# Performance work log

Measured on AMD Instinct MI355X. Metric: run time of the kernel, lower is better.

Reference implementation:

```python
import jax, jax.numpy as jnp
import numpy as np

B, T, C, H = 2048, 128, 256, 64

def setup_inputs() -> dict:
    key = jax.random.key(0)
    kx, kk, kq, kv = jax.random.split(key, 4)
    s = 1.0 / np.sqrt(C)  # nn.Linear default init scale (approx)
    return {
        "x": jax.random.normal(kx, (B, T, C), dtype=jnp.float32),
        "Wk": jax.random.uniform(kk, (C, H), jnp.float32, -s, s),
        "Wq": jax.random.uniform(kq, (C, H), jnp.float32, -s, s),
        "Wv": jax.random.uniform(kv, (C, H), jnp.float32, -s, s),
    }

def reference(x, Wk, Wq, Wv):
    # x: [B,T,C]; projections to [B,T,H]
    k = jnp.einsum('btc,ch->bth', x, Wk)
    q = jnp.einsum('btc,ch->bth', x, Wq)
    v = jnp.einsum('btc,ch->bth', x, Wv)
    # NOTE: original scales by C**-0.5 (input dim), not head_size**-0.5
    scale = jnp.asarray(C, x.dtype) ** -0.5
    wei = jnp.einsum('bth,bsh->bts', q, k) * scale  # [B,T,T]
    causal = jnp.tril(jnp.ones((T, T), dtype=bool))
    wei = jnp.where(causal, wei, -jnp.inf)
    wei = jax.nn.softmax(wei, axis=-1)
    # dropout is identity in eval mode (deterministic reference)
    return jnp.einsum('bts,bsh->bth', wei, v)
```

## Files before the change

kernel.cpp:

```cpp
#include <hip/hip_runtime.h>

typedef __bf16 bf16;
typedef __bf16 bf16x4 __attribute__((ext_vector_type(4)));
typedef __bf16 bf16x8 __attribute__((ext_vector_type(8)));
typedef float  f32x4  __attribute__((ext_vector_type(4)));

#define B_ 2048
#define T_ 128
#define C_ 256
#define H_ 64

#define SMEM_BYTES 54272

__global__ void wt_kernel(const float* __restrict__ Wk, const float* __restrict__ Wq,
                          const float* __restrict__ Wv, bf16* __restrict__ Wt) {
    int o = blockIdx.x * 256 + threadIdx.x;
    int slot = o >> 14;
    int r    = o & 16383;
    int cc   = r >> 6;
    int h    = r & 63;
    const float* src = (slot == 0) ? Wq : (slot == 1 ? Wk : Wv);
    Wt[slot * 16384 + h * 256 + cc] = (bf16)src[r];
}

__global__ void __launch_bounds__(256, 3)
attn_kernel(const float* __restrict__ xg, const bf16* __restrict__ Wt,
            float* __restrict__ outg) {
    __shared__ __align__(16) char smem_raw[SMEM_BYTES];
    bf16* Qs  = (bf16*)smem_raw;
    bf16* Ks  = (bf16*)(smem_raw + 18432);
    bf16* Vt  = (bf16*)(smem_raw + 36864);
    bf16* Ps  = (bf16*)smem_raw;

    const int tid  = threadIdx.x;
    const int b    = blockIdx.x;
    const int w    = tid >> 6;
    const int lane = tid & 63;
    const int quad = lane >> 4;
    const int n16  = lane & 15;

    const f32x4 zero4 = {0.f, 0.f, 0.f, 0.f};
    const float*  xbp = xg + (size_t)b * (T_ * C_);
    const ushort* WtU = (const ushort*)Wt;

    f32x4 acc[2][12];
    #pragma unroll
    for (int mt = 0; mt < 2; mt++)
        #pragma unroll
        for (int nt = 0; nt < 12; nt++) acc[mt][nt] = zero4;

    #pragma unroll
    for (int ks = 0; ks < 8; ks++) {
        bf16x8 a[2];
        #pragma unroll
        for (int mt = 0; mt < 2; mt++) {
            const float* ap = xbp + (16 * (2 * w + mt) + n16) * C_ + ks * 32 + 8 * quad;
            float4 a0 = *(const float4*)(ap);
            float4 a1 = *(const float4*)(ap + 4);
            bf16x8 av = {(bf16)a0.x, (bf16)a0.y, (bf16)a0.z, (bf16)a0.w,
                         (bf16)a1.x, (bf16)a1.y, (bf16)a1.z, (bf16)a1.w};
            a[mt] = av;
        }
        #pragma unroll
        for (int nt = 0; nt < 12; nt++) {
            const ushort* wp = WtU + (nt >> 2) * 16384 + (16 * (nt & 3) + n16) * 256 + ks * 32 + 8 * quad;
            bf16x8 bfr = *(const bf16x8*)wp;
            acc[0][nt] = __builtin_amdgcn_mfma_f32_16x16x32_bf16(a[0], bfr, acc[0][nt], 0, 0, 0);
            acc[1][nt] = __builtin_amdgcn_mfma_f32_16x16x32_bf16(a[1], bfr, acc[1][nt], 0, 0, 0);
        }
    }

    #pragma unroll
    for (int mt = 0; mt < 2; mt++) {
        int tbase = 16 * (2 * w + mt) + 4 * quad;
        #pragma unroll
        for (int nt = 0; nt < 4; nt++) {
            int h = 16 * nt + n16;
            #pragma unroll
            for (int r = 0; r < 4; r++)
                Qs[(tbase + r) * 72 + h] = (bf16)(acc[mt][nt][r] * 0.0625f);
        }
        #pragma unroll
        for (int nt = 4; nt < 8; nt++) {
            int h = 16 * (nt & 3) + n16;
            #pragma unroll
            for (int r = 0; r < 4; r++)
                Ks[(tbase + r) * 72 + h] = (bf16)acc[mt][nt][r];
        }
        #pragma unroll
        for (int nt = 8; nt < 12; nt++) {
            int h = 16 * (nt - 8) + n16;
            bf16x4 pv = {(bf16)acc[mt][nt][0], (bf16)acc[mt][nt][1],
                         (bf16)acc[mt][nt][2], (bf16)acc[mt][nt][3]};
            *(bf16x4*)(Vt + h * 136 + tbase) = pv;
        }
    }
    __syncthreads();

    f32x4 sacc[2][8];
    int mts[2] = {w, 7 - w};
    #pragma unroll
    for (int half = 0; half < 2; half++) {
        int mt = mts[half];
        int sT = ((mt >> 1) + 1) * 2;
        bf16x8 qa[2];
        #pragma unroll
        for (int ks = 0; ks < 2; ks++)
            qa[ks] = *(const bf16x8*)(Qs + (16 * mt + n16) * 72 + 32 * ks + 8 * quad);
        #pragma unroll
        for (int nt = 0; nt < 8; nt++) {
            sacc[half][nt] = zero4;
            if (nt < sT) {
                bf16x8 kb0 = *(const bf16x8*)(Ks + (16 * nt + n16) * 72 + 8 * quad);
                bf16x8 kb1 = *(const bf16x8*)(Ks + (16 * nt + n16) * 72 + 32 + 8 * quad);
                sacc[half][nt] = __builtin_amdgcn_mfma_f32_16x16x32_bf16(qa[0], kb0, sacc[half][nt], 0, 0, 0);
                sacc[half][nt] = __builtin_amdgcn_mfma_f32_16x16x32_bf16(qa[1], kb1, sacc[half][nt], 0, 0, 0);
            }
        }
        #pragma unroll
        for (int r = 0; r < 4; r++) {
            int t = 16 * mt + 4 * quad + r;
            float mx = -3.0e38f;
            #pragma unroll
            for (int nt = 0; nt < 8; nt++) {
                if (nt < sT) {
                    float v = sacc[half][nt][r];
                    v = (16 * nt + n16 <= t) ? v : -3.0e38f;
                    sacc[half][nt][r] = v;
                    mx = fmaxf(mx, v);
                }
            }
            mx = fmaxf(mx, __shfl_xor(mx, 1));
            mx = fmaxf(mx, __shfl_xor(mx, 2));
            mx = fmaxf(mx, __shfl_xor(mx, 4));
            mx = fmaxf(mx, __shfl_xor(mx, 8));
            float sum = 0.f;
            #pragma unroll
            for (int nt = 0; nt < 8; nt++) {
                if (nt < sT) {
                    float p = __builtin_amdgcn_exp2f((sacc[half][nt][r] - mx) * 1.4426950408889634f);
                    sacc[half][nt][r] = p;
                    sum += p;
                }
            }
            sum += __shfl_xor(sum, 1);
            sum += __shfl_xor(sum, 2);
            sum += __shfl_xor(sum, 4);
            sum += __shfl_xor(sum, 8);
            float rinv = 1.0f / sum;
            #pragma unroll
            for (int nt = 0; nt < 8; nt++)
                if (nt < sT) sacc[half][nt][r] *= rinv;
        }
    }
    __syncthreads();

    #pragma unroll
    for (int half = 0; half < 2; half++) {
        int mt = mts[half];
        int sT = ((mt >> 1) + 1) * 2;
        #pragma unroll
        for (int nt = 0; nt < 8; nt++) {
            if (nt < sT) {
                #pragma unroll
                for (int r = 0; r < 4; r++)
                    Ps[(16 * mt + 4 * quad + r) * 136 + 16 * nt + n16] = (bf16)sacc[half][nt][r];
            }
        }
    }
    __syncthreads();

    f32x4 oacc[2][4];
    #pragma unroll
    for (int half = 0; half < 2; half++) {
        int mt  = mts[half];
        int kst = (mt >> 1) + 1;
        #pragma unroll
        for (int nt = 0; nt < 4; nt++) oacc[half][nt] = zero4;
        #pragma unroll
        for (int ks = 0; ks < 4; ks++) {
            if (ks < kst) {
                bf16x8 pa = *(const bf16x8*)(Ps + (16 * mt + n16) * 136 + 32 * ks + 8 * quad);
                #pragma unroll
                for (int nt = 0; nt < 4; nt++) {
                    bf16x8 vb = *(const bf16x8*)(Vt + (16 * nt + n16) * 136 + 32 * ks + 8 * quad);
                    oacc[half][nt] = __builtin_amdgcn_mfma_f32_16x16x32_bf16(pa, vb, oacc[half][nt], 0, 0, 0);
                }
            }
        }
    }
    #pragma unroll
    for (int half = 0; half < 2; half++) {
        int mt = mts[half];
        float* ob = outg + ((size_t)b * T_ + 16 * mt + 4 * quad) * H_;
        #pragma unroll
        for (int nt = 0; nt < 4; nt++)
            #pragma unroll
            for (int r = 0; r < 4; r++)
                ob[r * H_ + 16 * nt + n16] = oacc[half][nt][r];
    }
}

extern "C" void kernel_launch(void* const* d_in, const int* in_sizes, int n_in,
                              void* d_out, int out_size, void* d_ws, size_t ws_size,
                              hipStream_t stream) {
    const float* x  = (const float*)d_in[0];
    const float* Wk = (const float*)d_in[1];
    const float* Wq = (const float*)d_in[2];
    const float* Wv = (const float*)d_in[3];
    bf16* Wt = (bf16*)d_ws;
    wt_kernel<<<192, 256, 0, stream>>>(Wk, Wq, Wv, Wt);
    attn_kernel<<<B_, 256, 0, stream>>>(x, Wt, (float*)d_out);
}
```

Measured before the change: 500.3 us.

## Split QKV projection into two passes with x prefetch and tighter LDS padding

The projection now runs in two passes of six output tiles each instead of twelve at once, halving live accumulators, and software-prefetches the next k-slice of x one step ahead. The LDS row strides drop from 72/136 to 68/132, shrinking shared memory and changing the bank mapping. The output store is fused into the per-half PV loop to cut accumulator lifetime. In exchange, x is read twice from global/L2 and the new padding may introduce LDS bank conflicts.

```diff
diff --git a/kernel.cpp b/kernel.cpp
--- a/kernel.cpp
+++ b/kernel.cpp
@@ -10,7 +10,9 @@
 #define C_ 256
 #define H_ 64
 
-#define SMEM_BYTES 54272
+#define LDQ 68
+#define LDV 132
+#define SMEM_BYTES 51712
 
 __global__ void wt_kernel(const float* __restrict__ Wk, const float* __restrict__ Wq,
                           const float* __restrict__ Wv, bf16* __restrict__ Wt) {
@@ -28,8 +30,8 @@
             float* __restrict__ outg) {
     __shared__ __align__(16) char smem_raw[SMEM_BYTES];
     bf16* Qs  = (bf16*)smem_raw;
-    bf16* Ks  = (bf16*)(smem_raw + 18432);
-    bf16* Vt  = (bf16*)(smem_raw + 36864);
+    bf16* Ks  = (bf16*)(smem_raw + 17408);
+    bf16* Vt  = (bf16*)(smem_raw + 34816);
     bf16* Ps  = (bf16*)smem_raw;
 
     const int tid  = threadIdx.x;
@@ -43,56 +45,69 @@
     const float*  xbp = xg + (size_t)b * (T_ * C_);
     const ushort* WtU = (const ushort*)Wt;
 
-    f32x4 acc[2][12];
-    #pragma unroll
-    for (int mt = 0; mt < 2; mt++)
-        #pragma unroll
-        for (int nt = 0; nt < 12; nt++) acc[mt][nt] = zero4;
-
-    #pragma unroll
-    for (int ks = 0; ks < 8; ks++) {
-        bf16x8 a[2];
+    const float* xr0 = xbp + (32 * w + n16) * C_ + 8 * quad;
+    const float* xr1 = xr0 + 16 * C_;
+
+    #pragma unroll
+    for (int pass = 0; pass < 2; pass++) {
+        f32x4 acc[2][6];
+        #pragma unroll
+        for (int mt = 0; mt < 2; mt++)
+            #pragma unroll
+            for (int nt = 0; nt < 6; nt++) acc[mt][nt] = zero4;
+
+        float4 c00 = *(const float4*)(xr0);
+        float4 c01 = *(const float4*)(xr0 + 4);
+        float4 c10 = *(const float4*)(xr1);
+        float4 c11 = *(const float4*)(xr1 + 4);
+
+        #pragma unroll
+        for (int ks = 0; ks < 8; ks++) {
+            float4 n00, n01, n10, n11;
+            if (ks < 7) {
+                n00 = *(const float4*)(xr0 + (ks + 1) * 32);
+                n01 = *(const float4*)(xr0 + (ks + 1) * 32 + 4);
+                n10 = *(const float4*)(xr1 + (ks + 1) * 32);
+                n11 = *(const float4*)(xr1 + (ks + 1) * 32 + 4);
+            }
+            bf16x8 a0 = {(bf16)c00.x, (bf16)c00.y, (bf16)c00.z, (bf16)c00.w,
+                         (bf16)c01.x, (bf16)c01.y, (bf16)c01.z, (bf16)c01.w};
+            bf16x8 a1 = {(bf16)c10.x, (bf16)c10.y, (bf16)c10.z, (bf16)c10.w,
+                         (bf16)c11.x, (bf16)c11.y, (bf16)c11.z, (bf16)c11.w};
+            #pragma unroll
+            for (int nt = 0; nt < 6; nt++) {
+                int ntg = pass * 6 + nt;
+                const ushort* wp = WtU + (ntg >> 2) * 16384 + (16 * (ntg & 3) + n16) * 256 + ks * 32 + 8 * quad;
+                bf16x8 bfr = *(const bf16x8*)wp;
+                acc[0][nt] = __builtin_amdgcn_mfma_f32_16x16x32_bf16(a0, bfr, acc[0][nt], 0, 0, 0);
+                acc[1][nt] = __builtin_amdgcn_mfma_f32_16x16x32_bf16(a1, bfr, acc[1][nt], 0, 0, 0);
+            }
+            if (ks < 7) { c00 = n00; c01 = n01; c10 = n10; c11 = n11; }
+        }
+
         #pragma unroll
         for (int mt = 0; mt < 2; mt++) {
-            const float* ap = xbp + (16 * (2 * w + mt) + n16) * C_ + ks * 32 + 8 * quad;
-            float4 a0 = *(const float4*)(ap);
-            float4 a1 = *(const float4*)(ap + 4);
-            bf16x8 av = {(bf16)a0.x, (bf16)a0.y, (bf16)a0.z, (bf16)a0.w,
-                         (bf16)a1.x, (bf16)a1.y, (bf16)a1.z, (bf16)a1.w};
-            a[mt] = av;
-        }
-        #pragma unroll
-        for (int nt = 0; nt < 12; nt++) {
-            const ushort* wp = WtU + (nt >> 2) * 16384 + (16 * (nt & 3) + n16) * 256 + ks * 32 + 8 * quad;
-            bf16x8 bfr = *(const bf16x8*)wp;
-            acc[0][nt] = __builtin_amdgcn_mfma_f32_16x16x32_bf16(a[0], bfr, acc[0][nt], 0, 0, 0);
-            acc[1][nt] = __builtin_amdgcn_mfma_f32_16x16x32_bf16(a[1], bfr, acc[1][nt], 0, 0, 0);
-        }
-    }
-
-    #pragma unroll
-    for (int mt = 0; mt < 2; mt++) {
-        int tbase = 16 * (2 * w + mt) + 4 * quad;
-        #pragma unroll
-        for (int nt = 0; nt < 4; nt++) {
-            int h = 16 * nt + n16;
-            #pragma unroll
-            for (int r = 0; r < 4; r++)
-                Qs[(tbase + r) * 72 + h] = (bf16)(acc[mt][nt][r] * 0.0625f);
-        }
-        #pragma unroll
-        for (int nt = 4; nt < 8; nt++) {
-            int h = 16 * (nt & 3) + n16;
-            #pragma unroll
-            for (int r = 0; r < 4; r++)
-                Ks[(tbase + r) * 72 + h] = (bf16)acc[mt][nt][r];
-        }
-        #pragma unroll
-        for (int nt = 8; nt < 12; nt++) {
-            int h = 16 * (nt - 8) + n16;
-            bf16x4 pv = {(bf16)acc[mt][nt][0], (bf16)acc[mt][nt][1],
-                         (bf16)acc[mt][nt][2], (bf16)acc[mt][nt][3]};
-            *(bf16x4*)(Vt + h * 136 + tbase) = pv;
+            int tbase = 16 * (2 * w + mt) + 4 * quad;
+            #pragma unroll
+            for (int nt = 0; nt < 6; nt++) {
+                int ntg = pass * 6 + nt;
+                if (ntg < 4) {
+                    int h = 16 * ntg + n16;
+                    #pragma unroll
+                    for (int r = 0; r < 4; r++)
+                        Qs[(tbase + r) * LDQ + h] = (bf16)(acc[mt][nt][r] * 0.0625f);
+                } else if (ntg < 8) {
+                    int h = 16 * (ntg - 4) + n16;
+                    #pragma unroll
+                    for (int r = 0; r < 4; r++)
+                        Ks[(tbase + r) * LDQ + h] = (bf16)acc[mt][nt][r];
+                } else {
+                    int h = 16 * (ntg - 8) + n16;
+                    bf16x4 pv = {(bf16)acc[mt][nt][0], (bf16)acc[mt][nt][1],
+                                 (bf16)acc[mt][nt][2], (bf16)acc[mt][nt][3]};
+                    *(bf16x4*)(Vt + h * LDV + tbase) = pv;
+                }
+            }
         }
     }
     __syncthreads();
@@ -106,13 +121,13 @@
         bf16x8 qa[2];
         #pragma unroll
         for (int ks = 0; ks < 2; ks++)
-            qa[ks] = *(const bf16x8*)(Qs + (16 * mt + n16) * 72 + 32 * ks + 8 * quad);
+            qa[ks] = *(const bf16x8*)(Qs + (16 * mt + n16) * LDQ + 32 * ks + 8 * quad);
         #pragma unroll
         for (int nt = 0; nt < 8; nt++) {
             sacc[half][nt] = zero4;
             if (nt < sT) {
-                bf16x8 kb0 = *(const bf16x8*)(Ks + (16 * nt + n16) * 72 + 8 * quad);
-                bf16x8 kb1 = *(const bf16x8*)(Ks + (16 * nt + n16) * 72 + 32 + 8 * quad);
+                bf16x8 kb0 = *(const bf16x8*)(Ks + (16 * nt + n16) * LDQ + 8 * quad);
+                bf16x8 kb1 = *(const bf16x8*)(Ks + (16 * nt + n16) * LDQ + 32 + 8 * quad);
                 sacc[half][nt] = __builtin_amdgcn_mfma_f32_16x16x32_bf16(qa[0], kb0, sacc[half][nt], 0, 0, 0);
                 sacc[half][nt] = __builtin_amdgcn_mfma_f32_16x16x32_bf16(qa[1], kb1, sacc[half][nt], 0, 0, 0);
             }
@@ -164,40 +179,36 @@
             if (nt < sT) {
                 #pragma unroll
                 for (int r = 0; r < 4; r++)
-                    Ps[(16 * mt + 4 * quad + r) * 136 + 16 * nt + n16] = (bf16)sacc[half][nt][r];
+                    Ps[(16 * mt + 4 * quad + r) * LDV + 16 * nt + n16] = (bf16)sacc[half][nt][r];
             }
         }
     }
     __syncthreads();
 
-    f32x4 oacc[2][4];
     #pragma unroll
     for (int half = 0; half < 2; half++) {
         int mt  = mts[half];
         int kst = (mt >> 1) + 1;
-        #pragma unroll
-        for (int nt = 0; nt < 4; nt++) oacc[half][nt] = zero4;
+        f32x4 oacc[4];
+        #pragma unroll
+        for (int nt = 0; nt < 4; nt++) oacc[nt] = zero4;
         #pragma unroll
         for (int ks = 0; ks < 4; ks++) {
             if (ks < kst) {
-                bf16x8 pa = *(const bf16x8*)(Ps + (16 * mt + n16) * 136 + 32 * ks + 8 * quad);
+                bf16x8 pa = *(const bf16x8*)(Ps + (16 * mt + n16) * LDV + 32 * ks + 8 * quad);
                 #pragma unroll
                 for (int nt = 0; nt < 4; nt++) {
-                    bf16x8 vb = *(const bf16x8*)(Vt + (16 * nt + n16) * 136 + 32 * ks + 8 * quad);
-                    oacc[half][nt] = __builtin_amdgcn_mfma_f32_16x16x32_bf16(pa, vb, oacc[half][nt], 0, 0, 0);
-                }
-            }
-        }
-    }
-    #pragma unroll
-    for (int half = 0; half < 2; half++) {
-        int mt = mts[half];
+                    bf16x8 vb = *(const bf16x8*)(Vt + (16 * nt + n16) * LDV + 32 * ks + 8 * quad);
+                    oacc[nt] = __builtin_amdgcn_mfma_f32_16x16x32_bf16(pa, vb, oacc[nt], 0, 0, 0);
+                }
+            }
+        }
         float* ob = outg + ((size_t)b * T_ + 16 * mt + 4 * quad) * H_;
         #pragma unroll
-        for (int nt = 0; nt < 4; nt++)
-            #pragma unroll
-            for (int r = 0; r < 4; r++)
-                ob[r * H_ + 16 * nt + n16] = oacc[half][nt][r];
+        for (int r = 0; r < 4; r++)
+            #pragma unroll
+            for (int nt = 0; nt < 4; nt++)
+                ob[r * H_ + 16 * nt + n16] = oacc[nt][r];
     }
 }
 
```

Result: no change. 508.7 us (+1.7%).
